# Optimization experiments

Measured on AMD Instinct MI355X. Metric: run time of the kernel, lower is better.

## Reference

```python
import jax, jax.numpy as jnp
import numpy as np

B, S, D = 2, 2048, 512
H = 8
G = 4
LAMBDA_INIT = 0.2  # 0.8 - 0.6*exp(-0.3*(layer_idx-1)) with layer_idx=1
EPS = 1e-5


def setup_inputs() -> dict:
    key = jax.random.key(0)
    ks = jax.random.split(key, 16)
    n = jax.random.normal
    return {
        "x": n(ks[0], (B, S, D), jnp.float32),
        "K1_w": n(ks[1], (D, D), jnp.float32) * 0.02,
        "K1_b": n(ks[2], (D,), jnp.float32) * 0.02,
        "Q1_w": n(ks[3], (D, D), jnp.float32) * 0.02,
        "K2_w": n(ks[4], (D, D), jnp.float32) * 0.02,
        "K2_b": n(ks[5], (D,), jnp.float32) * 0.02,
        "Q2_w": n(ks[6], (D, D), jnp.float32) * 0.02,
        "V_w": n(ks[7], (D, D), jnp.float32) * 0.02,
        "lambda_q1": n(ks[8], (H, 1), jnp.float32),
        "lambda_k1": n(ks[9], (H, 1), jnp.float32),
        "lambda_q2": n(ks[10], (H, 1), jnp.float32),
        "lambda_k2": n(ks[11], (H, 1), jnp.float32),
        "gn_w": jnp.ones((D,), jnp.float32),
        "gn_b": jnp.zeros((D,), jnp.float32),
        "out_w": n(ks[12], (D, D), jnp.float32) * 0.02,
        "out_b": n(ks[13], (D,), jnp.float32) * 0.02,
    }


def reference(x, K1_w, K1_b, Q1_w, K2_w, K2_b, Q2_w, V_w,
              lambda_q1, lambda_k1, lambda_q2, lambda_k2,
              gn_w, gn_b, out_w, out_b):
    b, s, d = x.shape
    hd = d // H

    def heads(t):  # (b,s,d) -> (b,H,s,hd)
        return t.reshape(b, s, H, hd).transpose(0, 2, 1, 3)

    q1 = heads(x @ Q1_w.T)
    k1 = heads(x @ K1_w.T + K1_b)
    q2 = heads(x @ Q2_w.T)
    k2 = heads(x @ K2_w.T + K2_b)
    v = heads(x @ V_w.T)

    scale = hd ** 0.5
    a1 = jax.nn.softmax(jnp.einsum('bhqd,bhkd->bhqk', q1, k1) / scale, axis=-1)
    a2 = jax.nn.softmax(jnp.einsum('bhqd,bhkd->bhqk', q2, k2) / scale, axis=-1)

    lam = (jnp.exp(lambda_q1 * lambda_k1)
           - jnp.exp(lambda_q2 * lambda_k2) + LAMBDA_INIT)  # (H,1)
    attn = a1 - lam.reshape(1, H, 1, 1) * a2

    o = jnp.einsum('bhqk,bhkd->bhqd', attn, v)
    o = o.transpose(0, 2, 1, 3).reshape(b, s, d)

    # GroupNorm over channels: input (b, d, s), groups G normalize over (d/G, s)
    xc = o.transpose(0, 2, 1).reshape(b, G, d // G, s)
    mu = xc.mean(axis=(2, 3), keepdims=True)
    var = xc.var(axis=(2, 3), keepdims=True)
    xn = ((xc - mu) * jax.lax.rsqrt(var + EPS)).reshape(b, d, s)
    xn = xn * gn_w[None, :, None] + gn_b[None, :, None]

    y = xn.transpose(0, 2, 1) @ out_w.T + out_b
    return y
```

## Files before the change

### kernel.cpp

```cpp
#include <hip/hip_runtime.h>
#include <hip/hip_bf16.h>

typedef __bf16 bf16;
typedef __attribute__((ext_vector_type(4))) __bf16 bf16x4;
typedef __attribute__((ext_vector_type(8))) __bf16 bf16x8;
typedef __attribute__((ext_vector_type(4))) float f32x4;

#define MFMA16(a, b, c) __builtin_amdgcn_mfma_f32_16x16x32_bf16((a), (b), (c), 0, 0, 0)

static constexpr float EPS = 1e-5f;
static constexpr float LAMBDA_INIT = 0.2f;
static constexpr float LOG2E = 1.44269504088896340736f;

__device__ __forceinline__ bf16x8 cvt8(const float* p) {
    const f32x4 a = *(const f32x4*)p;
    const f32x4 b = *(const f32x4*)(p + 4);
    bf16x8 r;
    r[0] = (bf16)a[0]; r[1] = (bf16)a[1]; r[2] = (bf16)a[2]; r[3] = (bf16)a[3];
    r[4] = (bf16)b[0]; r[5] = (bf16)b[1]; r[6] = (bf16)b[2]; r[7] = (bf16)b[3];
    return r;
}

__device__ __forceinline__ void gload_lds16(const void* g, void* l) {
    __builtin_amdgcn_global_load_lds(
        (const __attribute__((address_space(1))) unsigned int*)g,
        (__attribute__((address_space(3))) unsigned int*)l,
        16, 0, 0);
}

__global__ __launch_bounds__(256) void prep_kernel(
    const float* __restrict__ x,
    const float* __restrict__ q1w, const float* __restrict__ k1w,
    const float* __restrict__ q2w, const float* __restrict__ k2w,
    const float* __restrict__ vw,
    const float* __restrict__ ow, const float* __restrict__ gnw,
    const float* __restrict__ gnb,
    bf16* __restrict__ xb, bf16* __restrict__ wb,
    bf16* __restrict__ owg, float* __restrict__ S0, float* __restrict__ stats)
{
    const int tid = threadIdx.x;
    if (blockIdx.x < 1664) {
        const size_t base = ((size_t)blockIdx.x * 256 + tid) * 8;
        if (base < 2097152) {
            *(bf16x8*)(xb + base) = cvt8(x + base);
        } else {
            const size_t wbase = base - 2097152;
            const int wsel = (int)(wbase >> 18);
            const size_t off = wbase & 262143;
            const float* W = (wsel == 0) ? q1w : (wsel == 1) ? k1w :
                             (wsel == 2) ? q2w : (wsel == 3) ? k2w : vw;
            *(bf16x8*)(wb + wbase) = cvt8(W + off);
        }
        return;
    }

    __shared__ float red[4];
    const int pb = blockIdx.x - 1664;
    if (pb == 0 && tid < 16) stats[tid] = 0.f;

    const int n0 = pb * 16;
    const int c0 = tid, c1 = tid + 256;
    const float gw0 = gnw[c0], gw1 = gnw[c1];
    const float gb0 = gnb[c0], gb1 = gnb[c1];

    for (int n = 0; n < 16; ++n) {
        const size_t rowb = (size_t)(n0 + n) * 512;
        const float w0 = ow[rowb + c0];
        const float w1 = ow[rowb + c1];
        owg[rowb + c0] = (bf16)(w0 * gw0);
        owg[rowb + c1] = (bf16)(w1 * gw1);
        float s = gb0 * w0 + gb1 * w1;
#pragma unroll
        for (int off = 1; off < 64; off <<= 1) s += __shfl_xor(s, off, 64);
        if ((tid & 63) == 0) red[tid >> 6] = s;
        __syncthreads();
        if (tid == 0) S0[n0 + n] = red[0] + red[1] + red[2] + red[3];
        __syncthreads();
    }
}

__global__ __launch_bounds__(256) void proj_kernel(
    const bf16* __restrict__ xb, const bf16* __restrict__ wb,
    const float* __restrict__ k1b, const float* __restrict__ k2b,
    bf16* __restrict__ q1o, bf16* __restrict__ k1o,
    bf16* __restrict__ q2o, bf16* __restrict__ k2o,
    bf16* __restrict__ vto)
{
    __shared__ __align__(16) bf16 sh[32768];
    bf16* const As0 = sh;
    bf16* const As1 = sh + 8192;
    bf16* const Bs0 = sh + 16384;
    bf16* const Bs1 = sh + 24576;

    const int tid = threadIdx.x;
    const int wave = tid >> 6, lane = tid & 63;
    const int l15 = lane & 15, quad = lane >> 4;
    const int wm = wave >> 1, wn = wave & 1;

    const int mb = blockIdx.x / 20;
    const int nb = blockIdx.x % 20;
    const int wsel = nb >> 2;
    const int nrow0 = (nb & 3) * 128;

    const int srow = lane >> 3;
    const int scol = 8 * ((lane & 7) ^ srow);
    const bf16* ag = xb + (size_t)(mb * 128 + srow) * 512 + scol;
    const bf16* bg = wb + (size_t)(wsel * 512 + nrow0 + srow) * 512 + scol;

    f32x4 acc[4][4];
#pragma unroll
    for (int i = 0; i < 4; ++i)
#pragma unroll
        for (int j = 0; j < 4; ++j)
            acc[i][j] = (f32x4){0.f, 0.f, 0.f, 0.f};

#define STAGE_PROJ(abuf, bbuf, s) do {                                         \
    const int k0_ = (s) * 64;                                                  \
    _Pragma("unroll")                                                          \
    for (int c_ = 0; c_ < 4; ++c_) {                                           \
        const int chunk_ = wave * 4 + c_;                                      \
        gload_lds16(ag + (size_t)(chunk_ * 8) * 512 + k0_, (abuf) + chunk_ * 512); \
        gload_lds16(bg + (size_t)(chunk_ * 8) * 512 + k0_, (bbuf) + chunk_ * 512); \
    }                                                                          \
} while (0)

    STAGE_PROJ(As0, Bs0, 0);
    __syncthreads();

    const int ka = 8 * (quad ^ (l15 & 7));

    for (int s = 0; s < 8; ++s) {
        const bf16* Ac = (s & 1) ? As1 : As0;
        const bf16* Bc = (s & 1) ? Bs1 : Bs0;
        if (s < 7) {
            if (s & 1) STAGE_PROJ(As0, Bs0, s + 1);
            else       STAGE_PROJ(As1, Bs1, s + 1);
        }

        bf16x8 al[4], ah[4], bl[4], bh_[4];
#pragma unroll
        for (int i = 0; i < 4; ++i) {
            const bf16* p = Ac + (wm * 64 + i * 16 + l15) * 64;
            al[i] = *(const bf16x8*)(p + ka);
            ah[i] = *(const bf16x8*)(p + (ka ^ 32));
        }
#pragma unroll
        for (int j = 0; j < 4; ++j) {
            const bf16* p = Bc + (wn * 64 + j * 16 + l15) * 64;
            bl[j]  = *(const bf16x8*)(p + ka);
            bh_[j] = *(const bf16x8*)(p + (ka ^ 32));
        }

#pragma unroll
        for (int i = 0; i < 4; ++i)
#pragma unroll
            for (int j = 0; j < 4; ++j) {
                acc[i][j] = MFMA16(al[i], bl[j], acc[i][j]);
                acc[i][j] = MFMA16(ah[i], bh_[j], acc[i][j]);
            }

        __syncthreads();
    }

    const int bidx = mb >> 4;
    const int sbase = (mb & 15) * 128;
    const float scale = (wsel == 0 || wsel == 2) ? 0.125f * LOG2E : 1.0f;

    if (wsel != 4) {
        bf16* const T = sh;
        const int swzq = quad << 4;
#pragma unroll
        for (int j = 0; j < 4; ++j) {
            const int nl = wn * 64 + j * 16 + l15;
            const int ncol = nrow0 + nl;
            float bias = 0.f;
            if (wsel == 1) bias = k1b[ncol];
            if (wsel == 3) bias = k2b[ncol];
            const int nswz = nl ^ swzq;
#pragma unroll
            for (int i = 0; i < 4; ++i) {
                const int mbase = wm * 64 + i * 16 + quad * 4;
#pragma unroll
                for (int r = 0; r < 4; ++r)
                    T[(mbase + r) * 128 + nswz] = (bf16)(acc[i][j][r] * scale + bias);
            }
        }
        __syncthreads();

        bf16* const dst = (wsel == 0) ? q1o : (wsel == 1) ? k1o :
                          (wsel == 2) ? q2o : k2o;
#pragma unroll
        for (int hsel = 0; hsel < 2; ++hsel) {
            const int h = (nrow0 >> 6) + hsel;
            bf16* db = dst + ((size_t)(bidx * 8 + h) * 2048 + sbase) * 64;
#pragma unroll
            for (int ps = 0; ps < 4; ++ps) {
                const int idx = (ps * 256 + tid) * 8;
                const int m = idx >> 6, hd = idx & 63;
                const bf16x8 v = *(const bf16x8*)(
                    T + m * 128 + ((hsel * 64 + hd) ^ (((m >> 2) & 3) << 4)));
                *(bf16x8*)(db + idx) = v;
            }
        }
    } else {
        bf16* const Tt = sh;
#pragma unroll
        for (int j = 0; j < 4; ++j) {
            const int nl = wn * 64 + j * 16 + l15;
            const int hd = (nrow0 + nl) & 63;
            const int xh = (hd >> 1) & 3;
            const int swz = (nl & 7) << 2;
#pragma unroll
            for (int i = 0; i < 4; ++i) {
                const int colb = (wm * 64 + (i >> 1) * 32 + ((quad ^ xh) << 3)
                                  + ((i & 1) << 2)) ^ swz;
                bf16x4 pk;
#pragma unroll
                for (int r = 0; r < 4; ++r) pk[r] = (bf16)acc[i][j][r];
                *(bf16x4*)(Tt + nl * 132 + colb) = pk;
            }
        }
        __syncthreads();

#pragma unroll
        for (int ps = 0; ps < 8; ++ps) {
            const int rown = ps * 16 + (tid >> 4);
            const int seg = tid & 15;
            const int swz = (rown & 7) << 2;
            const bf16x4 lo = *(const bf16x4*)(Tt + rown * 132 + ((seg * 8) ^ swz));
            const bf16x4 hi = *(const bf16x4*)(Tt + rown * 132 + ((seg * 8 + 4) ^ swz));
            const int ncol = nrow0 + rown;
            const int h = ncol >> 6, hd = ncol & 63;
            bf16x8 v;
            v[0] = lo[0]; v[1] = lo[1]; v[2] = lo[2]; v[3] = lo[3];
            v[4] = hi[0]; v[5] = hi[1]; v[6] = hi[2]; v[7] = hi[3];
            *(bf16x8*)(vto + ((size_t)(bidx * 8 + h) * 64 + hd) * 2048
                       + sbase + seg * 8) = v;
        }
    }
#undef STAGE_PROJ
}

__global__ __launch_bounds__(512, 4) void attn_kernel(
    const bf16* __restrict__ q1, const bf16* __restrict__ k1,
    const bf16* __restrict__ q2, const bf16* __restrict__ k2,
    const bf16* __restrict__ vt,
    const float* __restrict__ lq1, const float* __restrict__ lk1,
    const float* __restrict__ lq2, const float* __restrict__ lk2,
    bf16* __restrict__ o, float* __restrict__ stats)
{
    __shared__ __align__(16) bf16 smem[2][12288];
    __shared__ float lbuf[8][2][16];
    __shared__ float sred[2][2];

    const int tid = threadIdx.x;
    const int wave = tid >> 6;
    const int lane = tid & 63;
    const int l15 = lane & 15, quad = lane >> 4;
    const int kg = wave >> 2;
    const int w4 = wave & 3;
    const int qp = w4 & 1;
    const int st = w4 >> 1;

    const int rid = (blockIdx.x & 7) * 64 + (blockIdx.x >> 3);
    const int bh = rid >> 5;
    const int qt = rid & 31;
    const int b = bh >> 3, h = bh & 7;

    const bf16* k1t = k1 + (size_t)bh * 2048 * 64;
    const bf16* k2t = k2 + (size_t)bh * 2048 * 64;
    const bf16* vtt = vt + (size_t)bh * 64 * 2048;

    const bf16* qs = st ? q2 : q1;
    const int qrowA = qt * 64 + qp * 32 + l15;
    const bf16* qpA = qs + ((size_t)bh * 2048 + qrowA) * 64 + quad * 8;
    const bf16x8 qA0 = *(const bf16x8*)(qpA);
    const bf16x8 qA1 = *(const bf16x8*)(qpA + 32);
    const bf16x8 qB0 = *(const bf16x8*)(qpA + 16 * 64);
    const bf16x8 qB1 = *(const bf16x8*)(qpA + 16 * 64 + 32);

    const int sw = wave & 3;
    const int skey0 = (wave < 4) ? 0 : 1024;
    const size_t ksrc0 = (size_t)(skey0 + sw * 8 + (lane >> 3)) * 64
                       + 8 * ((lane & 7) ^ (lane >> 3));
    const size_t vsrc0 = (size_t)(sw * 16 + (lane >> 2)) * 2048 + skey0 + (lane & 3) * 8;

#define STAGE_ATTN(buf, itv) do {                                   \
    const size_t koff_ = ksrc0 + (size_t)(itv) * 32 * 64;           \
    gload_lds16(k1t + koff_, (buf) + wave * 512);                   \
    gload_lds16(k2t + koff_, (buf) + 4096 + wave * 512);            \
    gload_lds16(vtt + vsrc0 + (itv) * 32, (buf) + 8192 + wave * 512); \
} while (0)

    const int koffa = 8 * (quad ^ (l15 & 7));
    const int koffb = 8 * ((quad + 4) ^ (l15 & 7));
    const int vsw = 8 * (quad ^ ((l15 >> 1) & 3));

    f32x4 OA[4], OB[4];
    float lA = 0.f, lB = 0.f;
#pragma unroll
    for (int t = 0; t < 4; ++t) {
        OA[t] = (f32x4){0.f, 0.f, 0.f, 0.f};
        OB[t] = (f32x4){0.f, 0.f, 0.f, 0.f};
    }

    STAGE_ATTN(smem[0], 0);
    __syncthreads();

    for (int it = 0; it < 32; ++it) {
        const bf16* sb = smem[it & 1];
        if (it < 31) STAGE_ATTN(smem[(it & 1) ^ 1], it + 1);

        const bf16* kr = sb + st * 4096 + kg * 2048;
        const bf16* vr = sb + 8192 + kg * 2048;

        const bf16x8 kt0a = *(const bf16x8*)(kr + l15 * 64 + koffa);
        const bf16x8 kt0b = *(const bf16x8*)(kr + l15 * 64 + koffb);
        const bf16x8 kt1a = *(const bf16x8*)(kr + (16 + l15) * 64 + koffa);
        const bf16x8 kt1b = *(const bf16x8*)(kr + (16 + l15) * 64 + koffb);
        const bf16x8 v0 = *(const bf16x8*)(vr + l15 * 32 + vsw);
        const bf16x8 v1 = *(const bf16x8*)(vr + (16 + l15) * 32 + vsw);
        const bf16x8 v2 = *(const bf16x8*)(vr + (32 + l15) * 32 + vsw);
        const bf16x8 v3 = *(const bf16x8*)(vr + (48 + l15) * 32 + vsw);

        const f32x4 z = (f32x4){0.f, 0.f, 0.f, 0.f};
        __builtin_amdgcn_s_setprio(1);
        f32x4 sA0 = MFMA16(kt0a, qA0, z);  sA0 = MFMA16(kt0b, qA1, sA0);
        f32x4 sA1 = MFMA16(kt1a, qA0, z);  sA1 = MFMA16(kt1b, qA1, sA1);
        f32x4 sB0 = MFMA16(kt0a, qB0, z);  sB0 = MFMA16(kt0b, qB1, sB0);
        f32x4 sB1 = MFMA16(kt1a, qB0, z);  sB1 = MFMA16(kt1b, qB1, sB1);
        __builtin_amdgcn_s_setprio(0);

        bf16x8 bA, bB;
#pragma unroll
        for (int r = 0; r < 4; ++r) {
            float e;
            e = __builtin_amdgcn_exp2f(sA0[r]); lA += e; bA[r]     = (bf16)e;
            e = __builtin_amdgcn_exp2f(sA1[r]); lA += e; bA[4 + r] = (bf16)e;
            e = __builtin_amdgcn_exp2f(sB0[r]); lB += e; bB[r]     = (bf16)e;
            e = __builtin_amdgcn_exp2f(sB1[r]); lB += e; bB[4 + r] = (bf16)e;
        }

        __builtin_amdgcn_s_setprio(1);
        OA[0] = MFMA16(v0, bA, OA[0]);
        OA[1] = MFMA16(v1, bA, OA[1]);
        OA[2] = MFMA16(v2, bA, OA[2]);
        OA[3] = MFMA16(v3, bA, OA[3]);
        OB[0] = MFMA16(v0, bB, OB[0]);
        OB[1] = MFMA16(v1, bB, OB[1]);
        OB[2] = MFMA16(v2, bB, OB[2]);
        OB[3] = MFMA16(v3, bB, OB[3]);
        __builtin_amdgcn_s_setprio(0);

        __syncthreads();
    }

    lA += __shfl_xor(lA, 16, 64);  lA += __shfl_xor(lA, 32, 64);
    lB += __shfl_xor(lB, 16, 64);  lB += __shfl_xor(lB, 32, 64);
    if (lane < 16) {
        lbuf[wave][0][lane] = lA;
        lbuf[wave][1][lane] = lB;
    }
    __syncthreads();

    f32x4* rb = (f32x4*)smem;
    if (kg == 1) {
        f32x4* dst = rb + w4 * 512;
#pragma unroll
        for (int t = 0; t < 4; ++t) {
            dst[t * 64 + lane]       = OA[t];
            dst[(4 + t) * 64 + lane] = OB[t];
        }
    }
    __syncthreads();
    if (kg == 0) {
        const f32x4* src = rb + w4 * 512;
#pragma unroll
        for (int t = 0; t < 4; ++t) {
            OA[t] += src[t * 64 + lane];
            OB[t] += src[(4 + t) * 64 + lane];
        }
    }
    __syncthreads();

    if (kg == 0 && st == 1) {
        f32x4* dst = rb + qp * 512;
#pragma unroll
        for (int t = 0; t < 4; ++t) {
            dst[t * 64 + lane]       = OA[t];
            dst[(4 + t) * 64 + lane] = OB[t];
        }
    }
    __syncthreads();

    float ssum = 0.f, ssq = 0.f;
    if (kg == 0 && st == 0) {
        const f32x4* src = rb + qp * 512;
        const float L1A = lA + lbuf[4 + qp][0][l15];
        const float L1B = lB + lbuf[4 + qp][1][l15];
        const float L2A = lbuf[2 + qp][0][l15] + lbuf[6 + qp][0][l15];
        const float L2B = lbuf[2 + qp][1][l15] + lbuf[6 + qp][1][l15];
        const float lam = __expf(lq1[h] * lk1[h]) - __expf(lq2[h] * lk2[h]) + LAMBDA_INIT;
        const float i1A = 1.f / L1A, i2A = lam / L2A;
        const float i1B = 1.f / L1B, i2B = lam / L2B;
        const size_t rowA = (size_t)(b * 2048 + qt * 64 + qp * 32 + l15) * 512 + h * 64;
        const size_t rowB = rowA + 16 * 512;
#pragma unroll
        for (int t = 0; t < 4; ++t) {
            const f32x4 o2A = src[t * 64 + lane];
            const f32x4 o2B = src[(4 + t) * 64 + lane];
#pragma unroll
            for (int r = 0; r < 4; ++r) {
                const float vA = OA[t][r] * i1A - o2A[r] * i2A;
                const float vB = OB[t][r] * i1B - o2B[r] * i2B;
                ssum += vA + vB;
                ssq += vA * vA + vB * vB;
                o[rowA + t * 16 + quad * 4 + r] = (bf16)vA;
                o[rowB + t * 16 + quad * 4 + r] = (bf16)vB;
            }
        }
    }
#pragma unroll
    for (int off = 1; off < 64; off <<= 1) {
        ssum += __shfl_xor(ssum, off, 64);
        ssq += __shfl_xor(ssq, off, 64);
    }
    if (kg == 0 && st == 0 && lane == 0) { sred[qp][0] = ssum; sred[qp][1] = ssq; }
    __syncthreads();
    if (tid == 0) {
        const float s0 = sred[0][0] + sred[1][0];
        const float s1 = sred[0][1] + sred[1][1];
        const int bg = b * 4 + (h >> 1);
        atomicAdd(&stats[bg * 2], s0);
        atomicAdd(&stats[bg * 2 + 1], s1);
    }
#undef STAGE_ATTN
}

__global__ __launch_bounds__(256) void out_gemm_kernel(
    const bf16* __restrict__ o, const bf16* __restrict__ owg,
    const float* __restrict__ S0, const float* __restrict__ stats,
    const float* __restrict__ ob, float* __restrict__ y)
{
    __shared__ __align__(16) bf16 sh[24576];

    const int tid = threadIdx.x;
    const int wave = tid >> 6, lane = tid & 63;
    const int l15 = lane & 15, quad = lane >> 4;

    const int mb = blockIdx.x >> 3;
    const int nb = blockIdx.x & 7;
    const int b = mb >> 5;

    const float N = 128.f * 2048.f;
    float mu[4], rs[4];
#pragma unroll
    for (int g = 0; g < 4; ++g) {
        const float m = stats[(b * 4 + g) * 2] / N;
        const float var = stats[(b * 4 + g) * 2 + 1] / N - m * m;
        mu[g] = m;
        rs[g] = rsqrtf(var + EPS);
    }

    const int srow = lane >> 3;
    const int scol = 8 * ((lane & 7) ^ srow);
    const bf16* ag = o + (size_t)(mb * 64 + srow) * 512 + scol;
    const bf16* bg = owg + (size_t)(nb * 64 + srow) * 512 + scol;

#define STAGE_OUT(abuf, bbuf, s) do {                                          \
    const int k0_ = (s) * 64;                                                  \
    _Pragma("unroll")                                                          \
    for (int c_ = 0; c_ < 2; ++c_) {                                           \
        const int chunk_ = wave * 2 + c_;                                      \
        gload_lds16(ag + (size_t)(chunk_ * 8) * 512 + k0_, (abuf) + chunk_ * 512); \
        gload_lds16(bg + (size_t)(chunk_ * 8) * 512 + k0_, (bbuf) + chunk_ * 512); \
    }                                                                          \
} while (0)

    f32x4 acc[4], tot[4];
#pragma unroll
    for (int i = 0; i < 4; ++i) {
        acc[i] = (f32x4){0.f, 0.f, 0.f, 0.f};
        tot[i] = (f32x4){0.f, 0.f, 0.f, 0.f};
    }
    float s1g[4];
    float s1p = 0.f;
#pragma unroll
    for (int g = 0; g < 4; ++g) s1g[g] = 0.f;

    STAGE_OUT(sh, sh + 12288, 0);
    STAGE_OUT(sh + 4096, sh + 12288 + 4096, 1);

    const int ka = 8 * (quad ^ (l15 & 7));

    int cur = 0;
    for (int kk = 0; kk < 8; ++kk) {
        if (kk < 7) {
            asm volatile("s_waitcnt vmcnt(4) lgkmcnt(0)\ns_barrier" ::: "memory");
        } else {
            asm volatile("s_waitcnt vmcnt(0) lgkmcnt(0)\ns_barrier" ::: "memory");
        }
        __builtin_amdgcn_sched_barrier(0);

        const bf16* Ac = sh + cur * 4096;
        const bf16* Bc = sh + 12288 + cur * 4096;
        const int n2 = (cur == 0) ? 2 : cur - 1;
        if (kk < 6) STAGE_OUT(sh + n2 * 4096, sh + 12288 + n2 * 4096, kk + 2);

        bf16x8 al[4], ah[4];
#pragma unroll
        for (int i = 0; i < 4; ++i) {
            const bf16* p = Ac + (i * 16 + l15) * 64;
            al[i] = *(const bf16x8*)(p + ka);
            ah[i] = *(const bf16x8*)(p + (ka ^ 32));
        }
        const bf16* pb = Bc + (wave * 16 + l15) * 64;
        const bf16x8 bl = *(const bf16x8*)(pb + ka);
        const bf16x8 bh = *(const bf16x8*)(pb + (ka ^ 32));

#pragma unroll
        for (int i = 0; i < 4; ++i) {
            acc[i] = MFMA16(al[i], bl, acc[i]);
            acc[i] = MFMA16(ah[i], bh, acc[i]);
        }

#pragma unroll
        for (int j = 0; j < 8; ++j) s1p += (float)bl[j] + (float)bh[j];

        if (kk & 1) {
            const int g = kk >> 1;
#pragma unroll
            for (int i = 0; i < 4; ++i) {
#pragma unroll
                for (int r = 0; r < 4; ++r) tot[i][r] += rs[g] * acc[i][r];
                acc[i] = (f32x4){0.f, 0.f, 0.f, 0.f};
            }
            float sg = s1p + __shfl_xor(s1p, 16, 64);
            sg += __shfl_xor(sg, 32, 64);
            s1g[g] = sg;
            s1p = 0.f;
        }

        cur = (cur == 2) ? 0 : cur + 1;
    }
    __syncthreads();

    const int ncol = nb * 64 + wave * 16 + l15;
    float bias = S0[ncol] + ob[ncol];
#pragma unroll
    for (int g = 0; g < 4; ++g) bias -= mu[g] * rs[g] * s1g[g];

    float* const Tf = (float*)sh;
    const int nl = wave * 16 + l15;
#pragma unroll
    for (int i = 0; i < 4; ++i) {
        const int mbase = i * 16 + quad * 4;
#pragma unroll
        for (int r = 0; r < 4; ++r)
            Tf[(mbase + r) * 64 + (nl ^ (quad << 4))] = tot[i][r] + bias;
    }
    __syncthreads();

#pragma unroll
    for (int ps = 0; ps < 4; ++ps) {
        const int idx = (ps * 256 + tid) * 4;
        const int m = idx >> 6, n4 = idx & 63;
        const f32x4 v = *(const f32x4*)(Tf + m * 64 + (n4 ^ (((m >> 2) & 3) << 4)));
        *(f32x4*)(y + (size_t)(mb * 64 + m) * 512 + nb * 64 + n4) = v;
    }
#undef STAGE_OUT
}

extern "C" void kernel_launch(void* const* d_in, const int* in_sizes, int n_in,
                              void* d_out, int out_size, void* d_ws, size_t ws_size,
                              hipStream_t stream)
{
    const float* x   = (const float*)d_in[0];
    const float* K1w = (const float*)d_in[1];
    const float* K1b = (const float*)d_in[2];
    const float* Q1w = (const float*)d_in[3];
    const float* K2w = (const float*)d_in[4];
    const float* K2b = (const float*)d_in[5];
    const float* Q2w = (const float*)d_in[6];
    const float* Vw  = (const float*)d_in[7];
    const float* lq1 = (const float*)d_in[8];
    const float* lk1 = (const float*)d_in[9];
    const float* lq2 = (const float*)d_in[10];
    const float* lk2 = (const float*)d_in[11];
    const float* gnw = (const float*)d_in[12];
    const float* gnb = (const float*)d_in[13];
    const float* Ow  = (const float*)d_in[14];
    const float* Ob  = (const float*)d_in[15];

    const size_t SZ = (size_t)2 * 8 * 2048 * 64;
    bf16* q1 = (bf16*)d_ws;
    bf16* k1 = q1 + SZ;
    bf16* q2 = k1 + SZ;
    bf16* k2 = q2 + SZ;
    bf16* vt = k2 + SZ;
    bf16* o  = vt + SZ;
    bf16* xb = o;
    bf16* wb = o + SZ;
    bf16* owg = wb + (size_t)2560 * 512;
    float* S0 = (float*)(owg + 512 * 512);
    float* stats = S0 + 512;

    prep_kernel<<<1696, 256, 0, stream>>>(x, Q1w, K1w, Q2w, K2w, Vw,
                                          Ow, gnw, gnb, xb, wb, owg, S0, stats);
    proj_kernel<<<640, 256, 0, stream>>>(xb, wb, K1b, K2b,
                                         q1, k1, q2, k2, vt);
    attn_kernel<<<512, 512, 0, stream>>>(q1, k1, q2, k2, vt,
                                         lq1, lk1, lq2, lk2, o, stats);
    out_gemm_kernel<<<512, 256, 0, stream>>>(o, owg, S0, stats, Ob,
                                             (float*)d_out);
}
```

Before: 171.5 us.

## Load K fragments directly to registers in attention and swizzle GEMM block order

The attention kernel stops staging K1/K2 tiles through LDS. Each wave now loads its own K fragments straight from global memory into registers, double-buffered across a two-step unrolled loop, and only V goes through LDS. This shrinks shared memory use and LDS traffic but adds redundant global loads of K that rely on cache. The projection and output GEMM kernels also remap block indices so that consecutive blocks land on different XCDs, aiming for better L2 locality.

```diff
diff --git a/kernel.cpp b/kernel.cpp
--- a/kernel.cpp
+++ b/kernel.cpp
@@ -97,8 +97,9 @@
     const int l15 = lane & 15, quad = lane >> 4;
     const int wm = wave >> 1, wn = wave & 1;
 
-    const int mb = blockIdx.x / 20;
-    const int nb = blockIdx.x % 20;
+    const int swzb = (blockIdx.x & 7) * 80 + (blockIdx.x >> 3);
+    const int mb = swzb / 20;
+    const int nb = swzb % 20;
     const int wsel = nb >> 2;
     const int nrow0 = (nb & 3) * 128;
 
@@ -249,9 +250,12 @@
     const float* __restrict__ lq2, const float* __restrict__ lk2,
     bf16* __restrict__ o, float* __restrict__ stats)
 {
-    __shared__ __align__(16) bf16 smem[2][12288];
+    __shared__ __align__(16) bf16 smem[16384];
     __shared__ float lbuf[8][2][16];
     __shared__ float sred[2][2];
+
+    bf16* const vb0 = smem;
+    bf16* const vb1 = smem + 4096;
 
     const int tid = threadIdx.x;
     const int wave = tid >> 6;
@@ -267,8 +271,7 @@
     const int qt = rid & 31;
     const int b = bh >> 3, h = bh & 7;
 
-    const bf16* k1t = k1 + (size_t)bh * 2048 * 64;
-    const bf16* k2t = k2 + (size_t)bh * 2048 * 64;
+    const bf16* kst = (st ? k2 : k1) + (size_t)bh * 2048 * 64;
     const bf16* vtt = vt + (size_t)bh * 64 * 2048;
 
     const bf16* qs = st ? q2 : q1;
@@ -279,21 +282,15 @@
     const bf16x8 qB0 = *(const bf16x8*)(qpA + 16 * 64);
     const bf16x8 qB1 = *(const bf16x8*)(qpA + 16 * 64 + 32);
 
+    const bf16* kpl = kst + (size_t)(kg * 1024 + l15) * 64 + quad * 8;
+
     const int sw = wave & 3;
     const int skey0 = (wave < 4) ? 0 : 1024;
-    const size_t ksrc0 = (size_t)(skey0 + sw * 8 + (lane >> 3)) * 64
-                       + 8 * ((lane & 7) ^ (lane >> 3));
     const size_t vsrc0 = (size_t)(sw * 16 + (lane >> 2)) * 2048 + skey0 + (lane & 3) * 8;
 
-#define STAGE_ATTN(buf, itv) do {                                   \
-    const size_t koff_ = ksrc0 + (size_t)(itv) * 32 * 64;           \
-    gload_lds16(k1t + koff_, (buf) + wave * 512);                   \
-    gload_lds16(k2t + koff_, (buf) + 4096 + wave * 512);            \
-    gload_lds16(vtt + vsrc0 + (itv) * 32, (buf) + 8192 + wave * 512); \
-} while (0)
-
-    const int koffa = 8 * (quad ^ (l15 & 7));
-    const int koffb = 8 * ((quad + 4) ^ (l15 & 7));
+#define STAGE_V(buf, itv) \
+    gload_lds16(vtt + vsrc0 + (itv) * 32, (buf) + wave * 512)
+
     const int vsw = 8 * (quad ^ ((l15 >> 1) & 3));
 
     f32x4 OA[4], OB[4];
@@ -304,54 +301,72 @@
         OB[t] = (f32x4){0.f, 0.f, 0.f, 0.f};
     }
 
-    STAGE_ATTN(smem[0], 0);
-    __syncthreads();
-
-    for (int it = 0; it < 32; ++it) {
-        const bf16* sb = smem[it & 1];
-        if (it < 31) STAGE_ATTN(smem[(it & 1) ^ 1], it + 1);
-
-        const bf16* kr = sb + st * 4096 + kg * 2048;
-        const bf16* vr = sb + 8192 + kg * 2048;
-
-        const bf16x8 kt0a = *(const bf16x8*)(kr + l15 * 64 + koffa);
-        const bf16x8 kt0b = *(const bf16x8*)(kr + l15 * 64 + koffb);
-        const bf16x8 kt1a = *(const bf16x8*)(kr + (16 + l15) * 64 + koffa);
-        const bf16x8 kt1b = *(const bf16x8*)(kr + (16 + l15) * 64 + koffb);
-        const bf16x8 v0 = *(const bf16x8*)(vr + l15 * 32 + vsw);
-        const bf16x8 v1 = *(const bf16x8*)(vr + (16 + l15) * 32 + vsw);
-        const bf16x8 v2 = *(const bf16x8*)(vr + (32 + l15) * 32 + vsw);
-        const bf16x8 v3 = *(const bf16x8*)(vr + (48 + l15) * 32 + vsw);
-
-        const f32x4 z = (f32x4){0.f, 0.f, 0.f, 0.f};
-        __builtin_amdgcn_s_setprio(1);
-        f32x4 sA0 = MFMA16(kt0a, qA0, z);  sA0 = MFMA16(kt0b, qA1, sA0);
-        f32x4 sA1 = MFMA16(kt1a, qA0, z);  sA1 = MFMA16(kt1b, qA1, sA1);
-        f32x4 sB0 = MFMA16(kt0a, qB0, z);  sB0 = MFMA16(kt0b, qB1, sB0);
-        f32x4 sB1 = MFMA16(kt1a, qB0, z);  sB1 = MFMA16(kt1b, qB1, sB1);
-        __builtin_amdgcn_s_setprio(0);
-
-        bf16x8 bA, bB;
-#pragma unroll
-        for (int r = 0; r < 4; ++r) {
-            float e;
-            e = __builtin_amdgcn_exp2f(sA0[r]); lA += e; bA[r]     = (bf16)e;
-            e = __builtin_amdgcn_exp2f(sA1[r]); lA += e; bA[4 + r] = (bf16)e;
-            e = __builtin_amdgcn_exp2f(sB0[r]); lB += e; bB[r]     = (bf16)e;
-            e = __builtin_amdgcn_exp2f(sB1[r]); lB += e; bB[4 + r] = (bf16)e;
-        }
-
-        __builtin_amdgcn_s_setprio(1);
-        OA[0] = MFMA16(v0, bA, OA[0]);
-        OA[1] = MFMA16(v1, bA, OA[1]);
-        OA[2] = MFMA16(v2, bA, OA[2]);
-        OA[3] = MFMA16(v3, bA, OA[3]);
-        OB[0] = MFMA16(v0, bB, OB[0]);
-        OB[1] = MFMA16(v1, bB, OB[1]);
-        OB[2] = MFMA16(v2, bB, OB[2]);
-        OB[3] = MFMA16(v3, bB, OB[3]);
-        __builtin_amdgcn_s_setprio(0);
-
+    bf16x8 kA0, kA1, kA2, kA3, kB0, kB1, kB2, kB3;
+
+    kA0 = *(const bf16x8*)(kpl);
+    kA1 = *(const bf16x8*)(kpl + 32);
+    kA2 = *(const bf16x8*)(kpl + 1024);
+    kA3 = *(const bf16x8*)(kpl + 1056);
+    STAGE_V(vb0, 0);
+    __syncthreads();
+
+#define ATTN_BODY(KF0, KF1, KF2, KF3, VB)                                     \
+    do {                                                                      \
+        const bf16* vr = (VB) + kg * 2048;                                    \
+        const bf16x8 v0 = *(const bf16x8*)(vr + l15 * 32 + vsw);              \
+        const bf16x8 v1 = *(const bf16x8*)(vr + (16 + l15) * 32 + vsw);       \
+        const bf16x8 v2 = *(const bf16x8*)(vr + (32 + l15) * 32 + vsw);       \
+        const bf16x8 v3 = *(const bf16x8*)(vr + (48 + l15) * 32 + vsw);       \
+        const f32x4 z = (f32x4){0.f, 0.f, 0.f, 0.f};                          \
+        __builtin_amdgcn_s_setprio(1);                                        \
+        f32x4 sA0 = MFMA16(KF0, qA0, z);  sA0 = MFMA16(KF1, qA1, sA0);        \
+        f32x4 sA1 = MFMA16(KF2, qA0, z);  sA1 = MFMA16(KF3, qA1, sA1);        \
+        f32x4 sB0 = MFMA16(KF0, qB0, z);  sB0 = MFMA16(KF1, qB1, sB0);        \
+        f32x4 sB1 = MFMA16(KF2, qB0, z);  sB1 = MFMA16(KF3, qB1, sB1);        \
+        __builtin_amdgcn_s_setprio(0);                                        \
+        bf16x8 bA, bB;                                                        \
+        _Pragma("unroll")                                                     \
+        for (int r = 0; r < 4; ++r) {                                         \
+            float e;                                                          \
+            e = __builtin_amdgcn_exp2f(sA0[r]); lA += e; bA[r]     = (bf16)e; \
+            e = __builtin_amdgcn_exp2f(sA1[r]); lA += e; bA[4 + r] = (bf16)e; \
+            e = __builtin_amdgcn_exp2f(sB0[r]); lB += e; bB[r]     = (bf16)e; \
+            e = __builtin_amdgcn_exp2f(sB1[r]); lB += e; bB[4 + r] = (bf16)e; \
+        }                                                                     \
+        __builtin_amdgcn_s_setprio(1);                                        \
+        OA[0] = MFMA16(v0, bA, OA[0]);                                        \
+        OA[1] = MFMA16(v1, bA, OA[1]);                                        \
+        OA[2] = MFMA16(v2, bA, OA[2]);                                        \
+        OA[3] = MFMA16(v3, bA, OA[3]);                                        \
+        OB[0] = MFMA16(v0, bB, OB[0]);                                        \
+        OB[1] = MFMA16(v1, bB, OB[1]);                                        \
+        OB[2] = MFMA16(v2, bB, OB[2]);                                        \
+        OB[3] = MFMA16(v3, bB, OB[3]);                                        \
+        __builtin_amdgcn_s_setprio(0);                                        \
+    } while (0)
+
+    for (int it2 = 0; it2 < 16; ++it2) {
+        const int itE = it2 * 2;
+        {
+            const bf16* kn = kpl + (size_t)(itE + 1) * 2048;
+            kB0 = *(const bf16x8*)(kn);
+            kB1 = *(const bf16x8*)(kn + 32);
+            kB2 = *(const bf16x8*)(kn + 1024);
+            kB3 = *(const bf16x8*)(kn + 1056);
+            STAGE_V(vb1, itE + 1);
+        }
+        ATTN_BODY(kA0, kA1, kA2, kA3, vb0);
+        __syncthreads();
+
+        if (itE + 2 < 32) {
+            const bf16* kn = kpl + (size_t)(itE + 2) * 2048;
+            kA0 = *(const bf16x8*)(kn);
+            kA1 = *(const bf16x8*)(kn + 32);
+            kA2 = *(const bf16x8*)(kn + 1024);
+            kA3 = *(const bf16x8*)(kn + 1056);
+            STAGE_V(vb0, itE + 2);
+        }
+        ATTN_BODY(kB0, kB1, kB2, kB3, vb1);
         __syncthreads();
     }
 
@@ -434,7 +449,8 @@
         atomicAdd(&stats[bg * 2], s0);
         atomicAdd(&stats[bg * 2 + 1], s1);
     }
-#undef STAGE_ATTN
+#undef STAGE_V
+#undef ATTN_BODY
 }
 
 __global__ __launch_bounds__(256) void out_gemm_kernel(
@@ -448,8 +464,9 @@
     const int wave = tid >> 6, lane = tid & 63;
     const int l15 = lane & 15, quad = lane >> 4;
 
-    const int mb = blockIdx.x >> 3;
-    const int nb = blockIdx.x & 7;
+    const int swzb = (blockIdx.x & 7) * 64 + (blockIdx.x >> 3);
+    const int mb = swzb >> 3;
+    const int nb = swzb & 7;
     const int b = mb >> 5;
 
     const float N = 128.f * 2048.f;
```

Result: slower. 273.1 us (+59.3%).

## Fuse fp32-to-bf16 conversion into projection and output GEMM loads, drop prep kernel

Applied to the files above, without the earlier changes.

Removes the separate prep kernel. The projection GEMM now reads fp32 x and weights directly, converts them to bf16 in registers and writes them to LDS. The output GEMM now scales out_w by the GroupNorm weight in its loader and computes the GroupNorm-bias row sums inline. Block indices are also swizzled across XCDs in both GEMMs. This saves a kernel launch and a round trip of bf16 copies through global memory. In exchange, the async global-to-LDS loads become synchronous register loads, the out GEMM drops from a 3-stage to a 2-stage pipeline with extra barriers, and each block converts the weights redundantly.

```diff
diff --git a/kernel.cpp b/kernel.cpp
--- a/kernel.cpp
+++ b/kernel.cpp
@@ -28,63 +28,15 @@
         16, 0, 0);
 }
 
-__global__ __launch_bounds__(256) void prep_kernel(
+__global__ __launch_bounds__(256) void proj_kernel(
     const float* __restrict__ x,
     const float* __restrict__ q1w, const float* __restrict__ k1w,
     const float* __restrict__ q2w, const float* __restrict__ k2w,
     const float* __restrict__ vw,
-    const float* __restrict__ ow, const float* __restrict__ gnw,
-    const float* __restrict__ gnb,
-    bf16* __restrict__ xb, bf16* __restrict__ wb,
-    bf16* __restrict__ owg, float* __restrict__ S0, float* __restrict__ stats)
-{
-    const int tid = threadIdx.x;
-    if (blockIdx.x < 1664) {
-        const size_t base = ((size_t)blockIdx.x * 256 + tid) * 8;
-        if (base < 2097152) {
-            *(bf16x8*)(xb + base) = cvt8(x + base);
-        } else {
-            const size_t wbase = base - 2097152;
-            const int wsel = (int)(wbase >> 18);
-            const size_t off = wbase & 262143;
-            const float* W = (wsel == 0) ? q1w : (wsel == 1) ? k1w :
-                             (wsel == 2) ? q2w : (wsel == 3) ? k2w : vw;
-            *(bf16x8*)(wb + wbase) = cvt8(W + off);
-        }
-        return;
-    }
-
-    __shared__ float red[4];
-    const int pb = blockIdx.x - 1664;
-    if (pb == 0 && tid < 16) stats[tid] = 0.f;
-
-    const int n0 = pb * 16;
-    const int c0 = tid, c1 = tid + 256;
-    const float gw0 = gnw[c0], gw1 = gnw[c1];
-    const float gb0 = gnb[c0], gb1 = gnb[c1];
-
-    for (int n = 0; n < 16; ++n) {
-        const size_t rowb = (size_t)(n0 + n) * 512;
-        const float w0 = ow[rowb + c0];
-        const float w1 = ow[rowb + c1];
-        owg[rowb + c0] = (bf16)(w0 * gw0);
-        owg[rowb + c1] = (bf16)(w1 * gw1);
-        float s = gb0 * w0 + gb1 * w1;
-#pragma unroll
-        for (int off = 1; off < 64; off <<= 1) s += __shfl_xor(s, off, 64);
-        if ((tid & 63) == 0) red[tid >> 6] = s;
-        __syncthreads();
-        if (tid == 0) S0[n0 + n] = red[0] + red[1] + red[2] + red[3];
-        __syncthreads();
-    }
-}
-
-__global__ __launch_bounds__(256) void proj_kernel(
-    const bf16* __restrict__ xb, const bf16* __restrict__ wb,
     const float* __restrict__ k1b, const float* __restrict__ k2b,
     bf16* __restrict__ q1o, bf16* __restrict__ k1o,
     bf16* __restrict__ q2o, bf16* __restrict__ k2o,
-    bf16* __restrict__ vto)
+    bf16* __restrict__ vto, float* __restrict__ stats)
 {
     __shared__ __align__(16) bf16 sh[32768];
     bf16* const As0 = sh;
@@ -93,19 +45,25 @@
     bf16* const Bs1 = sh + 24576;
 
     const int tid = threadIdx.x;
+    if (blockIdx.x == 0 && tid < 16) stats[tid] = 0.f;
+
     const int wave = tid >> 6, lane = tid & 63;
     const int l15 = lane & 15, quad = lane >> 4;
     const int wm = wave >> 1, wn = wave & 1;
 
-    const int mb = blockIdx.x / 20;
-    const int nb = blockIdx.x % 20;
+    const int swzb = (blockIdx.x & 7) * 80 + (blockIdx.x >> 3);
+    const int mb = swzb / 20;
+    const int nb = swzb % 20;
     const int wsel = nb >> 2;
     const int nrow0 = (nb & 3) * 128;
 
+    const float* W = (wsel == 0) ? q1w : (wsel == 1) ? k1w :
+                     (wsel == 2) ? q2w : (wsel == 3) ? k2w : vw;
+
     const int srow = lane >> 3;
     const int scol = 8 * ((lane & 7) ^ srow);
-    const bf16* ag = xb + (size_t)(mb * 128 + srow) * 512 + scol;
-    const bf16* bg = wb + (size_t)(wsel * 512 + nrow0 + srow) * 512 + scol;
+    const float* ag = x + (size_t)(mb * 128 + srow) * 512 + scol;
+    const float* bg = W + (size_t)(nrow0 + srow) * 512 + scol;
 
     f32x4 acc[4][4];
 #pragma unroll
@@ -119,8 +77,10 @@
     _Pragma("unroll")                                                          \
     for (int c_ = 0; c_ < 4; ++c_) {                                           \
         const int chunk_ = wave * 4 + c_;                                      \
-        gload_lds16(ag + (size_t)(chunk_ * 8) * 512 + k0_, (abuf) + chunk_ * 512); \
-        gload_lds16(bg + (size_t)(chunk_ * 8) * 512 + k0_, (bbuf) + chunk_ * 512); \
+        *(bf16x8*)((abuf) + chunk_ * 512 + lane * 8) =                         \
+            cvt8(ag + (size_t)(chunk_ * 8) * 512 + k0_);                       \
+        *(bf16x8*)((bbuf) + chunk_ * 512 + lane * 8) =                         \
+            cvt8(bg + (size_t)(chunk_ * 8) * 512 + k0_);                       \
     }                                                                          \
 } while (0)
 
@@ -438,18 +398,25 @@
 }
 
 __global__ __launch_bounds__(256) void out_gemm_kernel(
-    const bf16* __restrict__ o, const bf16* __restrict__ owg,
-    const float* __restrict__ S0, const float* __restrict__ stats,
-    const float* __restrict__ ob, float* __restrict__ y)
+    const bf16* __restrict__ o, const float* __restrict__ ow,
+    const float* __restrict__ gnw, const float* __restrict__ gnb,
+    const float* __restrict__ stats, const float* __restrict__ ob,
+    float* __restrict__ y)
 {
-    __shared__ __align__(16) bf16 sh[24576];
+    __shared__ __align__(16) bf16 sh[16384];
+    __shared__ float s0l[64];
+    bf16* const As0 = sh;
+    bf16* const As1 = sh + 4096;
+    bf16* const Bs0 = sh + 8192;
+    bf16* const Bs1 = sh + 12288;
 
     const int tid = threadIdx.x;
     const int wave = tid >> 6, lane = tid & 63;
     const int l15 = lane & 15, quad = lane >> 4;
 
-    const int mb = blockIdx.x >> 3;
-    const int nb = blockIdx.x & 7;
+    const int swzb = (blockIdx.x & 7) * 64 + (blockIdx.x >> 3);
+    const int mb = swzb >> 3;
+    const int nb = swzb & 7;
     const int b = mb >> 5;
 
     const float N = 128.f * 2048.f;
@@ -465,15 +432,45 @@
     const int srow = lane >> 3;
     const int scol = 8 * ((lane & 7) ^ srow);
     const bf16* ag = o + (size_t)(mb * 64 + srow) * 512 + scol;
-    const bf16* bg = owg + (size_t)(nb * 64 + srow) * 512 + scol;
+    const float* bgf = ow + (size_t)(nb * 64 + srow) * 512 + scol;
+
+    float s0a = 0.f, s0b = 0.f;
 
 #define STAGE_OUT(abuf, bbuf, s) do {                                          \
     const int k0_ = (s) * 64;                                                  \
-    _Pragma("unroll")                                                          \
-    for (int c_ = 0; c_ < 2; ++c_) {                                           \
-        const int chunk_ = wave * 2 + c_;                                      \
-        gload_lds16(ag + (size_t)(chunk_ * 8) * 512 + k0_, (abuf) + chunk_ * 512); \
-        gload_lds16(bg + (size_t)(chunk_ * 8) * 512 + k0_, (bbuf) + chunk_ * 512); \
+    const f32x4 gv0 = *(const f32x4*)(gnw + k0_ + scol);                       \
+    const f32x4 gv1 = *(const f32x4*)(gnw + k0_ + scol + 4);                   \
+    const f32x4 nb0 = *(const f32x4*)(gnb + k0_ + scol);                       \
+    const f32x4 nb1 = *(const f32x4*)(gnb + k0_ + scol + 4);                   \
+    gload_lds16(ag + (size_t)((wave * 2) * 8) * 512 + k0_,                     \
+                (abuf) + (wave * 2) * 512);                                    \
+    gload_lds16(ag + (size_t)((wave * 2 + 1) * 8) * 512 + k0_,                 \
+                (abuf) + (wave * 2 + 1) * 512);                                \
+    {                                                                          \
+        const float* p = bgf + (size_t)((wave * 2) * 8) * 512 + k0_;           \
+        const f32x4 w0 = *(const f32x4*)p;                                     \
+        const f32x4 w1 = *(const f32x4*)(p + 4);                               \
+        bf16x8 bv;                                                             \
+        _Pragma("unroll")                                                      \
+        for (int j_ = 0; j_ < 4; ++j_) {                                       \
+            bv[j_]     = (bf16)(w0[j_] * gv0[j_]);                             \
+            bv[4 + j_] = (bf16)(w1[j_] * gv1[j_]);                             \
+            s0a += nb0[j_] * w0[j_] + nb1[j_] * w1[j_];                        \
+        }                                                                      \
+        *(bf16x8*)((bbuf) + (wave * 2) * 512 + lane * 8) = bv;                 \
+    }                                                                          \
+    {                                                                          \
+        const float* p = bgf + (size_t)((wave * 2 + 1) * 8) * 512 + k0_;       \
+        const f32x4 w0 = *(const f32x4*)p;                                     \
+        const f32x4 w1 = *(const f32x4*)(p + 4);                               \
+        bf16x8 bv;                                                             \
+        _Pragma("unroll")                                                      \
+        for (int j_ = 0; j_ < 4; ++j_) {                                       \
+            bv[j_]     = (bf16)(w0[j_] * gv0[j_]);                             \
+            bv[4 + j_] = (bf16)(w1[j_] * gv1[j_]);                             \
+            s0b += nb0[j_] * w0[j_] + nb1[j_] * w1[j_];                        \
+        }                                                                      \
+        *(bf16x8*)((bbuf) + (wave * 2 + 1) * 512 + lane * 8) = bv;             \
     }                                                                          \
 } while (0)
 
@@ -488,24 +485,18 @@
 #pragma unroll
     for (int g = 0; g < 4; ++g) s1g[g] = 0.f;
 
-    STAGE_OUT(sh, sh + 12288, 0);
-    STAGE_OUT(sh + 4096, sh + 12288 + 4096, 1);
+    STAGE_OUT(As0, Bs0, 0);
+    __syncthreads();
 
     const int ka = 8 * (quad ^ (l15 & 7));
 
-    int cur = 0;
     for (int kk = 0; kk < 8; ++kk) {
+        const bf16* Ac = (kk & 1) ? As1 : As0;
+        const bf16* Bc = (kk & 1) ? Bs1 : Bs0;
         if (kk < 7) {
-            asm volatile("s_waitcnt vmcnt(4) lgkmcnt(0)\ns_barrier" ::: "memory");
-        } else {
-            asm volatile("s_waitcnt vmcnt(0) lgkmcnt(0)\ns_barrier" ::: "memory");
-        }
-        __builtin_amdgcn_sched_barrier(0);
-
-        const bf16* Ac = sh + cur * 4096;
-        const bf16* Bc = sh + 12288 + cur * 4096;
-        const int n2 = (cur == 0) ? 2 : cur - 1;
-        if (kk < 6) STAGE_OUT(sh + n2 * 4096, sh + 12288 + n2 * 4096, kk + 2);
+            if (kk & 1) STAGE_OUT(As0, Bs0, kk + 1);
+            else        STAGE_OUT(As1, Bs1, kk + 1);
+        }
 
         bf16x8 al[4], ah[4];
 #pragma unroll
@@ -526,6 +517,8 @@
 
 #pragma unroll
         for (int j = 0; j < 8; ++j) s1p += (float)bl[j] + (float)bh[j];
+
+        __syncthreads();
 
         if (kk & 1) {
             const int g = kk >> 1;
@@ -540,18 +533,23 @@
             s1g[g] = sg;
             s1p = 0.f;
         }
-
-        cur = (cur == 2) ? 0 : cur + 1;
-    }
-    __syncthreads();
-
-    const int ncol = nb * 64 + wave * 16 + l15;
-    float bias = S0[ncol] + ob[ncol];
+    }
+
+    s0a += __shfl_xor(s0a, 1, 64); s0a += __shfl_xor(s0a, 2, 64); s0a += __shfl_xor(s0a, 4, 64);
+    s0b += __shfl_xor(s0b, 1, 64); s0b += __shfl_xor(s0b, 2, 64); s0b += __shfl_xor(s0b, 4, 64);
+    if ((lane & 7) == 0) {
+        s0l[(wave * 2) * 8 + srow]     = s0a;
+        s0l[(wave * 2 + 1) * 8 + srow] = s0b;
+    }
+    __syncthreads();
+
+    const int nl = wave * 16 + l15;
+    const int ncol = nb * 64 + nl;
+    float bias = s0l[nl] + ob[ncol];
 #pragma unroll
     for (int g = 0; g < 4; ++g) bias -= mu[g] * rs[g] * s1g[g];
 
     float* const Tf = (float*)sh;
-    const int nl = wave * 16 + l15;
 #pragma unroll
     for (int i = 0; i < 4; ++i) {
         const int mbase = i * 16 + quad * 4;
@@ -599,18 +597,12 @@
     bf16* k2 = q2 + SZ;
     bf16* vt = k2 + SZ;
     bf16* o  = vt + SZ;
-    bf16* xb = o;
-    bf16* wb = o + SZ;
-    bf16* owg = wb + (size_t)2560 * 512;
-    float* S0 = (float*)(owg + 512 * 512);
-    float* stats = S0 + 512;
-
-    prep_kernel<<<1696, 256, 0, stream>>>(x, Q1w, K1w, Q2w, K2w, Vw,
-                                          Ow, gnw, gnb, xb, wb, owg, S0, stats);
-    proj_kernel<<<640, 256, 0, stream>>>(xb, wb, K1b, K2b,
-                                         q1, k1, q2, k2, vt);
+    float* stats = (float*)(o + SZ);
+
+    proj_kernel<<<640, 256, 0, stream>>>(x, Q1w, K1w, Q2w, K2w, Vw,
+                                         K1b, K2b, q1, k1, q2, k2, vt, stats);
     attn_kernel<<<512, 512, 0, stream>>>(q1, k1, q2, k2, vt,
                                          lq1, lk1, lq2, lk2, o, stats);
-    out_gemm_kernel<<<512, 256, 0, stream>>>(o, owg, S0, stats, Ob,
+    out_gemm_kernel<<<512, 256, 0, stream>>>(o, Ow, gnw, gnb, stats, Ob,
                                              (float*)d_out);
 }
```

Measured after the change: 180.7 us. 5.4% more time.
